# Optimization experiments

Hardware: AMD Instinct MI355X
Metric: run time of the kernel (lower is better)

## Reference

```python
import jax, jax.numpy as jnp
import numpy as np

N = 8192  # number of nodes


def _deg_norm(idx, n):
    # degree^{-1/2}, zero-degree clamped to 1 (DGL allow_zero_in_degree behavior)
    deg = jax.ops.segment_sum(jnp.ones(idx.shape[0], jnp.float32), idx, num_segments=n)
    return jax.lax.rsqrt(jnp.maximum(deg, 1.0))


def _graph_conv(h, src, dst, norm_src, norm_dst, W, b):
    # norm='both': scale at src, sparse sum-aggregate, scale at dst, then linear
    h = h * norm_src[:, None]
    m = jax.ops.segment_sum(h[src], dst, num_segments=h.shape[0])  # gather + scatter-add
    m = m * norm_dst[:, None]
    return m @ W + b


def setup_inputs() -> dict:
    key = jax.random.key(0)
    k = jax.random.split(key, 6)
    E = 262144
    x = jax.random.normal(k[0], (N, 256), jnp.float32)
    src = jax.random.randint(k[1], (E,), 0, N, jnp.int32)
    dst = jax.random.randint(k[2], (E,), 0, N, jnp.int32)
    W1 = jax.random.normal(k[3], (256, 128), jnp.float32) * (1.0 / np.sqrt(256))
    b1 = jnp.zeros((128,), jnp.float32)
    W2 = jax.random.normal(k[4], (128, 128), jnp.float32) * (1.0 / np.sqrt(128))
    b2 = jnp.zeros((128,), jnp.float32)
    return {"x": x, "src": src, "dst": dst, "W1": W1, "b1": b1, "W2": W2, "b2": b2}


def reference(x, src, dst, W1, b1, W2, b2):
    n = x.shape[0]
    norm_src = _deg_norm(src, n)  # out-degree norm
    norm_dst = _deg_norm(dst, n)  # in-degree norm
    # encode: GraphConv -> relu -> GraphConv  (dropout=0 -> identity)
    h = jax.nn.relu(_graph_conv(x, src, dst, norm_src, norm_dst, W1, b1))
    h = _graph_conv(h, src, dst, norm_src, norm_dst, W2, b2)
    # decode: sigmoid(h h^T), dense [N, N] reconstruction
    return jax.nn.sigmoid(h @ h.T)
```

## Files before the change

kernel.cpp:

```cpp
#include <hip/hip_runtime.h>
#include <hip/hip_bf16.h>

typedef __attribute__((ext_vector_type(8))) short short8;
typedef __attribute__((ext_vector_type(4))) float f32x4;

#define NNODES 8192
#define FDIM 128

static __device__ inline unsigned short f2bf(float f) {
    union { float f; unsigned int u; } a; a.f = f;
    unsigned int u = a.u;
    unsigned int r = u + 0x7FFFu + ((u >> 16) & 1u);
    return (unsigned short)(r >> 16);
}

__global__ void k_zero(int* __restrict__ p, int n) {
    int i = blockIdx.x * blockDim.x + threadIdx.x;
    if (i < n) p[i] = 0;
}

__global__ void k_deg_int(const int* __restrict__ src, const int* __restrict__ dst,
                          int* __restrict__ cnt, int E) {
    int e = blockIdx.x * blockDim.x + threadIdx.x;
    if (e < E) {
        atomicAdd(&cnt[src[e]], 1);
        atomicAdd(&cnt[NNODES + dst[e]], 1);
    }
}

__global__ __launch_bounds__(256) void k_scan_norms(const int* __restrict__ cnt,
                                                    float* __restrict__ norm_s,
                                                    int* __restrict__ row_start,
                                                    int* __restrict__ cursor, int n) {
    __shared__ int partial[256];
    __shared__ int offs[257];
    int t = threadIdx.x;
    int base = t * 32;
    const int* cnt_d = cnt + NNODES;
#pragma unroll
    for (int i = 0; i < 32; ++i)
        norm_s[base + i] = rsqrtf(fmaxf((float)cnt[base + i], 1.0f));
    int local[32];
    int s = 0;
#pragma unroll
    for (int i = 0; i < 32; ++i) { local[i] = s; s += cnt_d[base + i]; }
    partial[t] = s;
    __syncthreads();
    if (t == 0) {
        int acc = 0;
        for (int i = 0; i < 256; ++i) { offs[i] = acc; acc += partial[i]; }
        offs[256] = acc;
    }
    __syncthreads();
    int o = offs[t];
#pragma unroll
    for (int i = 0; i < 32; ++i) {
        int v = o + local[i];
        row_start[base + i] = v;
        cursor[base + i] = v;
    }
    if (t == 0) row_start[n] = offs[256];
}

__global__ void k_fill(const int* __restrict__ src, const int* __restrict__ dst,
                       int* __restrict__ cursor, int* __restrict__ csr_src, int E) {
    int e = blockIdx.x * blockDim.x + threadIdx.x;
    if (e < E) {
        int pos = atomicAdd(&cursor[dst[e]], 1);
        csr_src[pos] = src[e];
    }
}

template<int K>
__global__ __launch_bounds__(256) void k_lin(const float* __restrict__ X,
                                             const float* __restrict__ W,
                                             const float* __restrict__ norm,
                                             float* __restrict__ Y) {
    __shared__ float xs[16][K];
    int t = threadIdx.x;
    int row0 = blockIdx.x * 16;
    constexpr int K4 = K / 4;
    constexpr int NCH = 16 * K4 / 256;
#pragma unroll
    for (int i = 0; i < NCH; ++i) {
        int c = t + i * 256;
        int r = c / K4, k4 = c % K4;
        *(float4*)&xs[r][k4 * 4] = *(const float4*)(X + (size_t)(row0 + r) * K + k4 * 4);
    }
    __syncthreads();

    int lane = t & 31, g = t >> 5;
    int r0 = g * 2, r1 = r0 + 1;
    int c = lane * 4;
    f32x4 acc0 = {0.f, 0.f, 0.f, 0.f}, acc1 = {0.f, 0.f, 0.f, 0.f};
    for (int k = 0; k < K; k += 4) {
        f32x4 x0 = *(f32x4*)&xs[r0][k];
        f32x4 x1 = *(f32x4*)&xs[r1][k];
#pragma unroll
        for (int kk = 0; kk < 4; ++kk) {
            f32x4 w = *(const f32x4*)(W + (size_t)(k + kk) * FDIM + c);
            acc0 += w * x0[kk];
            acc1 += w * x1[kk];
        }
    }
    float n0 = norm[row0 + r0], n1 = norm[row0 + r1];
    *(f32x4*)(Y + (size_t)(row0 + r0) * FDIM + c) = acc0 * n0;
    *(f32x4*)(Y + (size_t)(row0 + r1) * FDIM + c) = acc1 * n1;
}

__global__ __launch_bounds__(256) void k_gatlin(const float* __restrict__ Y,
                                                const int* __restrict__ row_start,
                                                const int* __restrict__ csr_src,
                                                const float* __restrict__ b1,
                                                const float* __restrict__ W2,
                                                const float* __restrict__ norm_s,
                                                float* __restrict__ Y2) {
    __shared__ float h1s[8][132];
    const int t = threadIdx.x;
    const int g = t >> 5, lane = t & 31;
    const int node = blockIdx.x * 8 + g;
    const int c4 = lane << 2;

    int beg = row_start[node], end = row_start[node + 1];
    f32x4 acc0 = {0.f, 0.f, 0.f, 0.f}, acc1 = {0.f, 0.f, 0.f, 0.f};
    int e = beg;
    for (; e + 3 < end; e += 4) {
        int s0 = csr_src[e], s1 = csr_src[e + 1], s2 = csr_src[e + 2], s3 = csr_src[e + 3];
        f32x4 v0 = *(const f32x4*)(Y + ((size_t)s0 << 7) + c4);
        f32x4 v1 = *(const f32x4*)(Y + ((size_t)s1 << 7) + c4);
        f32x4 v2 = *(const f32x4*)(Y + ((size_t)s2 << 7) + c4);
        f32x4 v3 = *(const f32x4*)(Y + ((size_t)s3 << 7) + c4);
        acc0 += v0; acc1 += v1; acc0 += v2; acc1 += v3;
    }
    for (; e < end; ++e) {
        int s0 = csr_src[e];
        acc0 += *(const f32x4*)(Y + ((size_t)s0 << 7) + c4);
    }
    f32x4 acc = acc0 + acc1;
    float scale = rsqrtf(fmaxf((float)(end - beg), 1.0f));
    f32x4 b = *(const f32x4*)(b1 + c4);
    f32x4 v = acc * scale + b;
#pragma unroll
    for (int i = 0; i < 4; ++i) v[i] = fmaxf(v[i], 0.f);
    *(f32x4*)&h1s[g][c4] = v;
    __syncthreads();

    f32x4 acc2 = {0.f, 0.f, 0.f, 0.f};
    for (int k = 0; k < FDIM; k += 4) {
        f32x4 xv = *(f32x4*)&h1s[g][k];
#pragma unroll
        for (int kk = 0; kk < 4; ++kk) {
            f32x4 w = *(const f32x4*)(W2 + (size_t)(k + kk) * FDIM + c4);
            acc2 += w * xv[kk];
        }
    }
    float ns = norm_s[node];
    *(f32x4*)(Y2 + ((size_t)node << 7) + c4) = acc2 * ns;
}

__global__ __launch_bounds__(256) void k_gat2(const float* __restrict__ Y,
                                              const int* __restrict__ row_start,
                                              const int* __restrict__ csr_src,
                                              const float* __restrict__ bias,
                                              unsigned short* __restrict__ outp) {
    int t = threadIdx.x;
    int node = blockIdx.x * 8 + (t >> 5);
    int c4 = (t & 31) << 2;
    int beg = row_start[node], end = row_start[node + 1];
    f32x4 acc0 = {0.f, 0.f, 0.f, 0.f}, acc1 = {0.f, 0.f, 0.f, 0.f};
    int e = beg;
    for (; e + 3 < end; e += 4) {
        int s0 = csr_src[e], s1 = csr_src[e + 1], s2 = csr_src[e + 2], s3 = csr_src[e + 3];
        f32x4 v0 = *(const f32x4*)(Y + ((size_t)s0 << 7) + c4);
        f32x4 v1 = *(const f32x4*)(Y + ((size_t)s1 << 7) + c4);
        f32x4 v2 = *(const f32x4*)(Y + ((size_t)s2 << 7) + c4);
        f32x4 v3 = *(const f32x4*)(Y + ((size_t)s3 << 7) + c4);
        acc0 += v0; acc1 += v1; acc0 += v2; acc1 += v3;
    }
    for (; e < end; ++e) {
        int s0 = csr_src[e];
        acc0 += *(const f32x4*)(Y + ((size_t)s0 << 7) + c4);
    }
    f32x4 acc = acc0 + acc1;
    float scale = rsqrtf(fmaxf((float)(end - beg), 1.0f));
    f32x4 b = *(const f32x4*)(bias + c4);
    f32x4 v = acc * scale + b;
    ushort4 u;
    u.x = f2bf(v[0]); u.y = f2bf(v[1]); u.z = f2bf(v[2]); u.w = f2bf(v[3]);
    *(ushort4*)(outp + ((size_t)node << 7) + c4) = u;
}

__global__ __launch_bounds__(256) void k_decode(const __hip_bfloat16* __restrict__ H,
                                                float* __restrict__ C) {
    __shared__ __align__(16) unsigned char smem[65536];
    unsigned char* sA = smem;
    unsigned char* sB = smem + 32768;
    const int ti = blockIdx.x, tj = blockIdx.y;
    const int t = threadIdx.x;
    const unsigned char* gH = (const unsigned char*)H;

#pragma unroll
    for (int i = 0; i < 8; ++i) {
        int chunk = t + i * 256;
        int row = chunk >> 4;
        int cc = (chunk & 15) << 4;
        int lofs = row * 256 + (cc ^ ((row & 7) << 4));
        *(float4*)(sA + lofs) = *(const float4*)(gH + ((size_t)(ti * 128 + row) << 8) + cc);
        *(float4*)(sB + lofs) = *(const float4*)(gH + ((size_t)(tj * 128 + row) << 8) + cc);
    }
    __syncthreads();

    const int w = t >> 6, lane = t & 63;
    const int wr = (w >> 1) * 64, wc = (w & 1) * 64;
    const int lr = lane & 15;
    const int lk = (lane >> 4) * 16;

    f32x4 acc[4][4] = {};

#pragma unroll
    for (int ks = 0; ks < 4; ++ks) {
        short8 af[4], bfr[4];
#pragma unroll
        for (int mi = 0; mi < 4; ++mi) {
            int row = wr + mi * 16 + lr;
            int off = row * 256 + ((ks * 64 + lk) ^ ((row & 7) << 4));
            af[mi] = *(const short8*)(sA + off);
        }
#pragma unroll
        for (int ni = 0; ni < 4; ++ni) {
            int row = wc + ni * 16 + lr;
            int off = row * 256 + ((ks * 64 + lk) ^ ((row & 7) << 4));
            bfr[ni] = *(const short8*)(sB + off);
        }
#pragma unroll
        for (int mi = 0; mi < 4; ++mi)
#pragma unroll
            for (int ni = 0; ni < 4; ++ni)
                acc[mi][ni] = __builtin_amdgcn_mfma_f32_16x16x32_bf16(af[mi], bfr[ni],
                                                                      acc[mi][ni], 0, 0, 0);
    }

    const int rbase = (lane >> 4) * 4;
    const int cbase = lane & 15;
#pragma unroll
    for (int mi = 0; mi < 4; ++mi) {
        int rowb = ti * 128 + wr + mi * 16 + rbase;
#pragma unroll
        for (int ni = 0; ni < 4; ++ni) {
            int col = tj * 128 + wc + ni * 16 + cbase;
#pragma unroll
            for (int r = 0; r < 4; ++r) {
                float s = __builtin_amdgcn_rcpf(1.0f + __expf(-acc[mi][ni][r]));
                C[(size_t)(rowb + r) * NNODES + col] = s;
            }
        }
    }
}

extern "C" void kernel_launch(void* const* d_in, const int* in_sizes, int n_in,
                              void* d_out, int out_size, void* d_ws, size_t ws_size,
                              hipStream_t stream) {
    const float* x  = (const float*)d_in[0];
    const int* src  = (const int*)d_in[1];
    const int* dst  = (const int*)d_in[2];
    const float* W1 = (const float*)d_in[3];
    const float* b1 = (const float*)d_in[4];
    const float* W2 = (const float*)d_in[5];
    const float* b2 = (const float*)d_in[6];
    float* out = (float*)d_out;
    const int E = in_sizes[1];

    char* ws = (char*)d_ws;
    float* norm_s    = (float*)(ws + 0);
    int*   cnt       = (int*)(ws + (32 << 10));
    int*   row_start = (int*)(ws + (96 << 10));
    int*   cursor    = (int*)(ws + (132 << 10));
    int*   csr_src   = (int*)(ws + (164 << 10));
    char*  big       = ws + (164 << 10) + ((size_t)E * 4);
    float* bufA      = (float*)big;
    float* bufB      = (float*)(big + (4 << 20));
    __hip_bfloat16* h2bf = (__hip_bfloat16*)(big + (8 << 20));

    k_zero<<<64, 256, 0, stream>>>(cnt, 2 * NNODES);

    k_deg_int<<<(E + 255) / 256, 256, 0, stream>>>(src, dst, cnt, E);
    k_scan_norms<<<1, 256, 0, stream>>>(cnt, norm_s, row_start, cursor, NNODES);
    k_fill<<<(E + 255) / 256, 256, 0, stream>>>(src, dst, cursor, csr_src, E);

    k_lin<256><<<NNODES / 16, 256, 0, stream>>>(x, W1, norm_s, bufA);
    k_gatlin<<<NNODES / 8, 256, 0, stream>>>(bufA, row_start, csr_src, b1, W2, norm_s, bufB);
    k_gat2<<<NNODES / 8, 256, 0, stream>>>(bufB, row_start, csr_src, b2, (unsigned short*)h2bf);

    k_decode<<<dim3(64, 64), 256, 0, stream>>>(h2bf, out);
}
```

Before: 177.5 us.

## Merge CSR fill with first linear layer; vectorize decode output stores

The CSR fill kernel and the first dense linear kernel are combined into one launch, with blocks split by index into fill work and linear work, so the two independent stages can overlap and one launch is saved. In the decode kernel the MFMA operands are swapped so each lane holds four consecutive columns of the output tile, and the sigmoid results are written as one 16-byte vector store instead of four scalar strided stores. This is meant to cut store-instruction count and improve write coalescing on the large N×N output. It relies on the transposed accumulator layout being correct, since h·hᵀ is symmetric within the operand roles.

Result: no change. 179.1 us (median of 2 runs) (+0.9%).

```diff
diff --git a/kernel.cpp b/kernel.cpp
--- a/kernel.cpp
+++ b/kernel.cpp
@@ -62,23 +62,26 @@
     if (t == 0) row_start[n] = offs[256];
 }
 
-__global__ void k_fill(const int* __restrict__ src, const int* __restrict__ dst,
-                       int* __restrict__ cursor, int* __restrict__ csr_src, int E) {
-    int e = blockIdx.x * blockDim.x + threadIdx.x;
-    if (e < E) {
-        int pos = atomicAdd(&cursor[dst[e]], 1);
-        csr_src[pos] = src[e];
-    }
-}
-
-template<int K>
-__global__ __launch_bounds__(256) void k_lin(const float* __restrict__ X,
-                                             const float* __restrict__ W,
-                                             const float* __restrict__ norm,
-                                             float* __restrict__ Y) {
+__global__ __launch_bounds__(256) void k_fill_lin(const int* __restrict__ src,
+                                                  const int* __restrict__ dst,
+                                                  int* __restrict__ cursor,
+                                                  int* __restrict__ csr_src, int E, int fillB,
+                                                  const float* __restrict__ X,
+                                                  const float* __restrict__ W,
+                                                  const float* __restrict__ norm,
+                                                  float* __restrict__ Y) {
+    constexpr int K = 256;
     __shared__ float xs[16][K];
-    int t = threadIdx.x;
-    int row0 = blockIdx.x * 16;
+    const int t = threadIdx.x;
+    if (blockIdx.x < fillB) {
+        int e = blockIdx.x * 256 + t;
+        if (e < E) {
+            int pos = atomicAdd(&cursor[dst[e]], 1);
+            csr_src[pos] = src[e];
+        }
+        return;
+    }
+    int row0 = (blockIdx.x - fillB) * 16;
     constexpr int K4 = K / 4;
     constexpr int NCH = 16 * K4 / 256;
 #pragma unroll
@@ -88,7 +91,6 @@
         *(float4*)&xs[r][k4 * 4] = *(const float4*)(X + (size_t)(row0 + r) * K + k4 * 4);
     }
     __syncthreads();
-
     int lane = t & 31, g = t >> 5;
     int r0 = g * 2, r1 = r0 + 1;
     int c = lane * 4;
@@ -236,23 +238,23 @@
         for (int mi = 0; mi < 4; ++mi)
 #pragma unroll
             for (int ni = 0; ni < 4; ++ni)
-                acc[mi][ni] = __builtin_amdgcn_mfma_f32_16x16x32_bf16(af[mi], bfr[ni],
+                acc[mi][ni] = __builtin_amdgcn_mfma_f32_16x16x32_bf16(bfr[ni], af[mi],
                                                                       acc[mi][ni], 0, 0, 0);
     }
 
-    const int rbase = (lane >> 4) * 4;
-    const int cbase = lane & 15;
+    const int qrow = lane & 15;
+    const int pcolb = (lane >> 4) * 4;
 #pragma unroll
     for (int mi = 0; mi < 4; ++mi) {
-        int rowb = ti * 128 + wr + mi * 16 + rbase;
+        size_t rowoff = (size_t)(ti * 128 + wr + mi * 16 + qrow) * NNODES;
 #pragma unroll
         for (int ni = 0; ni < 4; ++ni) {
-            int col = tj * 128 + wc + ni * 16 + cbase;
-#pragma unroll
-            for (int r = 0; r < 4; ++r) {
-                float s = __builtin_amdgcn_rcpf(1.0f + __expf(-acc[mi][ni][r]));
-                C[(size_t)(rowb + r) * NNODES + col] = s;
-            }
+            int colb = tj * 128 + wc + ni * 16 + pcolb;
+            f32x4 s;
+#pragma unroll
+            for (int r = 0; r < 4; ++r)
+                s[r] = __builtin_amdgcn_rcpf(1.0f + __expf(-acc[mi][ni][r]));
+            *(f32x4*)(C + rowoff + colb) = s;
         }
     }
 }
@@ -285,9 +287,11 @@
 
     k_deg_int<<<(E + 255) / 256, 256, 0, stream>>>(src, dst, cnt, E);
     k_scan_norms<<<1, 256, 0, stream>>>(cnt, norm_s, row_start, cursor, NNODES);
-    k_fill<<<(E + 255) / 256, 256, 0, stream>>>(src, dst, cursor, csr_src, E);
-
-    k_lin<256><<<NNODES / 16, 256, 0, stream>>>(x, W1, norm_s, bufA);
+
+    const int fillB = (E + 255) / 256;
+    k_fill_lin<<<fillB + NNODES / 16, 256, 0, stream>>>(src, dst, cursor, csr_src, E, fillB,
+                                                        x, W1, norm_s, bufA);
+
     k_gatlin<<<NNODES / 8, 256, 0, stream>>>(bufA, row_start, csr_src, b1, W2, norm_s, bufB);
     k_gat2<<<NNODES / 8, 256, 0, stream>>>(bufB, row_start, csr_src, b2, (unsigned short*)h2bf);
 
```
